# Performance work log

Hardware: AMD Instinct MI355X
Metric: run time of the kernel (lower is better)

The kernel has to match this reference:

```python
import jax, jax.numpy as jnp
import numpy as np

MODEL_DIM = 512
STATE_DIM = 1024
ACTION_DIM = 1000
HEADS = 8
DIM_HEAD = MODEL_DIM // 8      # 64
LANDMARKS = MODEL_DIM // 2     # 256
PINV_ITERS = 6
CONV_K = 33                    # lucidrains residual_conv_kernel default
N_TOKENS = 16383               # seq becomes 16384 after cls token (multiple of LANDMARKS)


def layernorm(x, g, b, eps=1e-5):
    mu = jnp.mean(x, axis=-1, keepdims=True)
    var = jnp.var(x, axis=-1, keepdims=True)
    return (x - mu) * jax.lax.rsqrt(var + eps) * g + b


def moore_penrose_pinv(x, iters=PINV_ITERS):
    # x: [b, h, m, m]
    abs_x = jnp.abs(x)
    col = abs_x.sum(-1)
    row = abs_x.sum(-2)
    z = jnp.swapaxes(x, -1, -2) / (jnp.max(col) * jnp.max(row))
    I = jnp.eye(x.shape[-1], dtype=x.dtype)
    for _ in range(iters):
        xz = x @ z
        z = 0.25 * z @ (13 * I - xz @ (15 * I - xz @ (7 * I - xz)))
    return z


def nystrom_attention(x, qkv_W, conv_W, out_W, out_b):
    # x: [b, n, d]; n divisible by LANDMARKS (no padding branch needed)
    b, n, _ = x.shape
    scale = DIM_HEAD ** -0.5
    qkv = x @ qkv_W                                    # [b, n, 3*h*dh]
    q, k, v = jnp.split(qkv, 3, axis=-1)
    to_heads = lambda t: t.reshape(b, n, HEADS, DIM_HEAD).transpose(0, 2, 1, 3)
    q, k, v = to_heads(q), to_heads(k), to_heads(v)    # [b, h, n, dh]
    q = q * scale
    l = n // LANDMARKS
    q_l = q.reshape(b, HEADS, LANDMARKS, l, DIM_HEAD).mean(3)  # [b,h,m,dh]
    k_l = k.reshape(b, HEADS, LANDMARKS, l, DIM_HEAD).mean(3)
    sim1 = jnp.einsum('bhid,bhjd->bhij', q, k_l)       # [b,h,n,m]
    sim2 = jnp.einsum('bhid,bhjd->bhij', q_l, k_l)     # [b,h,m,m]
    sim3 = jnp.einsum('bhid,bhjd->bhij', q_l, k)       # [b,h,m,n]
    a1 = jax.nn.softmax(sim1, axis=-1)
    a2 = jax.nn.softmax(sim2, axis=-1)
    a3 = jax.nn.softmax(sim3, axis=-1)
    a2_inv = moore_penrose_pinv(a2)
    out = (a1 @ a2_inv) @ (a3 @ v)                     # [b,h,n,dh]
    # residual depthwise conv over sequence dim: treat [b,h,n,dh] as NCHW
    pad = CONV_K // 2
    out = out + jax.lax.conv_general_dilated(
        v, conv_W, window_strides=(1, 1), padding=((pad, pad), (0, 0)),
        dimension_numbers=('NCHW', 'OIHW', 'NCHW'), feature_group_count=HEADS)
    out = out.transpose(0, 2, 1, 3).reshape(b, n, HEADS * DIM_HEAD)
    return out @ out_W + out_b


def trans_layer(h, ln_g, ln_b, qkv_W, conv_W, out_W, out_b):
    # h: [n, d]
    x = h[None]
    x = x + nystrom_attention(layernorm(x, ln_g, ln_b), qkv_W, conv_W, out_W, out_b)
    return x[0]


def setup_inputs() -> dict:
    key = jax.random.key(0)
    ks = jax.random.split(key, 12)
    d = MODEL_DIM
    inp = {
        'h': jax.random.normal(ks[0], (N_TOKENS, STATE_DIM), jnp.float32),
        'W1': jax.random.normal(ks[1], (STATE_DIM, d), jnp.float32) * (STATE_DIM ** -0.5),
        'b1': jnp.zeros((d,), jnp.float32),
        'cls': jax.random.normal(ks[2], (1, d), jnp.float32),
        'ln1_g': jnp.ones((d,), jnp.float32), 'ln1_b': jnp.zeros((d,), jnp.float32),
        'qkv1_W': jax.random.normal(ks[3], (d, 3 * d), jnp.float32) * (d ** -0.5),
        'conv1_W': jax.random.normal(ks[4], (HEADS, 1, CONV_K, 1), jnp.float32) * 0.1,
        'out1_W': jax.random.normal(ks[5], (d, d), jnp.float32) * (d ** -0.5),
        'out1_b': jnp.zeros((d,), jnp.float32),
        'ln2_g': jnp.ones((d,), jnp.float32), 'ln2_b': jnp.zeros((d,), jnp.float32),
        'qkv2_W': jax.random.normal(ks[6], (d, 3 * d), jnp.float32) * (d ** -0.5),
        'conv2_W': jax.random.normal(ks[7], (HEADS, 1, CONV_K, 1), jnp.float32) * 0.1,
        'out2_W': jax.random.normal(ks[8], (d, d), jnp.float32) * (d ** -0.5),
        'out2_b': jnp.zeros((d,), jnp.float32),
        'lnf_g': jnp.ones((d,), jnp.float32), 'lnf_b': jnp.zeros((d,), jnp.float32),
        'fc2_W': jax.random.normal(ks[9], (d, ACTION_DIM), jnp.float32) * (d ** -0.5),
        'fc2_b': jnp.zeros((ACTION_DIM,), jnp.float32),
    }
    return inp


def reference(h, W1, b1, cls, ln1_g, ln1_b, qkv1_W, conv1_W, out1_W, out1_b,
              ln2_g, ln2_b, qkv2_W, conv2_W, out2_W, out2_b,
              lnf_g, lnf_b, fc2_W, fc2_b):
    x = jax.nn.relu(h @ W1 + b1)                 # [N, d]
    x = jnp.concatenate([cls, x], axis=0)        # [N+1, d] (16384)
    x = trans_layer(x, ln1_g, ln1_b, qkv1_W, conv1_W, out1_W, out1_b)
    x = trans_layer(x, ln2_g, ln2_b, qkv2_W, conv2_W, out2_W, out2_b)
    x = layernorm(x, lnf_g, lnf_b)[0]            # cls token
    return x @ fc2_W + fc2_b                     # [action_dim]
```

## Files before the change

kernel.cpp:

```cpp
#include <hip/hip_runtime.h>
#include <math.h>

typedef unsigned short u16;
typedef short bf16x8 __attribute__((ext_vector_type(8)));
typedef float f32x4 __attribute__((ext_vector_type(4)));

__device__ __forceinline__ u16 f2b(float x) {
    unsigned u = __builtin_bit_cast(unsigned, x);
    unsigned r = u + 0x7fffu + ((u >> 16) & 1u);
    return (u16)(r >> 16);
}
__device__ __forceinline__ float b2f(u16 v) {
    return __builtin_bit_cast(float, (unsigned)v << 16);
}
__device__ __forceinline__ void gl_lds16(const u16* g, u16* l) {
    __builtin_amdgcn_global_load_lds(
        (const __attribute__((address_space(1))) unsigned int*)g,
        (__attribute__((address_space(3))) unsigned int*)l, 16, 0, 0);
}
__device__ __forceinline__ float wred_sum(float v) {
#pragma unroll
    for (int o = 32; o > 0; o >>= 1) v += __shfl_down(v, o, 64);
    return v;
}
__device__ __forceinline__ float wred_max(float v) {
#pragma unroll
    for (int o = 32; o > 0; o >>= 1) v = fmaxf(v, __shfl_down(v, o, 64));
    return v;
}

struct GP {
    const u16* A; const u16* B; float* C;
    u16* Q; u16* Kb; u16* V;
    const float* bias;
    long sA, sB, sC;
    int K, ldc, tilesN;
};

template <int BM, int BN, int MODE>
__global__ __launch_bounds__(256) void mgemm(GP p) {
    constexpr int FR = BM / 32;
    constexpr int FC = BN / 32;
    constexpr int LA = BM / 64;
    constexpr int LB = BN / 64;
    __shared__ u16 As[2 * BM * 32] __attribute__((aligned(16)));
    __shared__ u16 Bs[2 * BN * 32] __attribute__((aligned(16)));

    int tid = threadIdx.x, lane = tid & 63, wave = tid >> 6;
    int wm = wave >> 1, wn = wave & 1;
    int nwg = gridDim.x, bid = blockIdx.x;
    int q = nwg >> 3, r = nwg & 7;
    int xcd = bid & 7, local = bid >> 3;
    int swz = (xcd < r ? xcd * (q + 1) : r * (q + 1) + (xcd - r) * q) + local;
    int tm = swz / p.tilesN, tn = swz % p.tilesN;
    int batch = blockIdx.y;
    int m0 = tm * BM, n0 = tn * BN;
    const u16* A = p.A + (long)batch * p.sA;
    const u16* B = p.B + (long)batch * p.sB;

    f32x4 acc[FR][FC];
#pragma unroll
    for (int i = 0; i < FR; i++)
#pragma unroll
        for (int j = 0; j < FC; j++) acc[i][j] = (f32x4){0.f, 0.f, 0.f, 0.f};

    int lr = lane & 15;
    int lcb = (lane >> 4) << 3;
    int quad = lane >> 4, cn = lane & 15;

    auto stage = [&](int buf, int k0) {
        u16* Ad = As + buf * (BM * 32);
        u16* Bd = Bs + buf * (BN * 32);
#pragma unroll
        for (int i = 0; i < LA; i++) {
            int chunk = wave * LA + i;
            gl_lds16(A + (long)(m0 + chunk * 16 + lr) * p.K + k0 + lcb,
                     Ad + chunk * 512 + lane * 8);
        }
#pragma unroll
        for (int i = 0; i < LB; i++) {
            int chunk = wave * LB + i;
            gl_lds16(B + (long)(n0 + chunk * 16 + lr) * p.K + k0 + lcb,
                     Bd + chunk * 512 + lane * 8);
        }
    };

    stage(0, 0);
    __syncthreads();
    int cur = 0;
    for (int k0 = 0; k0 < p.K; k0 += 32) {
        if (k0 + 32 < p.K) stage(cur ^ 1, k0 + 32);
        const u16* Asc = As + cur * (BM * 32);
        const u16* Bsc = Bs + cur * (BN * 32);
        bf16x8 af[FR], bfv[FC];
#pragma unroll
        for (int mi = 0; mi < FR; mi++)
            af[mi] = *(const bf16x8*)(Asc + (wm * FR + mi) * 512 + quad * 128 + cn * 8);
#pragma unroll
        for (int ni = 0; ni < FC; ni++)
            bfv[ni] = *(const bf16x8*)(Bsc + (wn * FC + ni) * 512 + quad * 128 + cn * 8);
#pragma unroll
        for (int mi = 0; mi < FR; mi++)
#pragma unroll
            for (int ni = 0; ni < FC; ni++)
                acc[mi][ni] = __builtin_amdgcn_mfma_f32_16x16x32_bf16(
                    af[mi], bfv[ni], acc[mi][ni], 0, 0, 0);
        __syncthreads();
        cur ^= 1;
    }

    if constexpr (MODE == 4) {
#pragma unroll
        for (int mi = 0; mi < FR; mi++) {
#pragma unroll
            for (int ni = 0; ni < FC; ni++) {
#pragma unroll
                for (int r = 0; r < 4; r++) {
                    int row = m0 + (wm * FR + mi) * 16 + quad * 4 + r;
                    int col = n0 + (wn * FC + ni) * 16 + cn;
                    float v = acc[mi][ni][r];
                    int h = col >> 6, d = col & 63;
                    if (col < 512)
                        p.Q[((long)h * 16384 + row) * 64 + d] = f2b(v * 0.125f);
                    else if (col < 1024)
                        p.Kb[((long)(h - 8) * 16384 + row) * 64 + d] = f2b(v);
                    else
                        p.V[((long)(h - 16) * 16384 + row) * 64 + d] = f2b(v);
                }
            }
        }
    } else {
        float* C = p.C + (long)batch * p.sC;
#pragma unroll
        for (int mi = 0; mi < FR; mi++) {
#pragma unroll
            for (int ni = 0; ni < FC; ni++) {
#pragma unroll
                for (int r = 0; r < 4; r++) {
                    int row = m0 + (wm * FR + mi) * 16 + quad * 4 + r;
                    int col = n0 + (wn * FC + ni) * 16 + cn;
                    float v = acc[mi][ni][r];
                    if (MODE == 0) {
                        C[(long)row * p.ldc + col] = v;
                    } else if (MODE == 1) {
                        C[(long)row * p.ldc + col] = fmaxf(v + p.bias[col], 0.f);
                    } else if (MODE == 2) {
                        C[(long)row * p.ldc + col] += v + p.bias[col];
                    }
                }
            }
        }
    }
}

template <int BM, int BN, int MODE>
static void launch_mgemm(hipStream_t st, GP p, int M, int N, int batch) {
    p.tilesN = N / BN;
    dim3 grid((M / BM) * (N / BN), batch);
    mgemm<BM, BN, MODE><<<grid, 256, 0, st>>>(p);
}

__global__ __launch_bounds__(512) void flash_a3v(
    const u16* __restrict__ QLb, const u16* __restrict__ Kb,
    const u16* __restrict__ VT, float* __restrict__ PART) {
    __shared__ u16 QLs[16384] __attribute__((aligned(16)));
    __shared__ u16 Ks[4096] __attribute__((aligned(16)));
    __shared__ u16 Vs[4096] __attribute__((aligned(16)));
    __shared__ u16 Ps[16384] __attribute__((aligned(16)));
    int tid = threadIdx.x, lane = tid & 63, w = tid >> 6;
    int head = blockIdx.y, split = blockIdx.x;
    const u16* QLh = QLb + (long)head * 256 * 64;
    const u16* Kh = Kb + ((long)head * 16384 + split * 512) * 64;
    const u16* Vh = VT + (long)head * 64 * 16384 + split * 512;
    int quad = lane >> 4, cn = lane & 15;
    int lr = lane & 15, lc = (lane >> 4) << 3;

    for (int c = w; c < 32; c += 8) {
        int rc = c >> 1, kc = c & 1;
        gl_lds16(QLh + (long)(rc * 16 + lr) * 64 + kc * 32 + lc, QLs + c * 512 + lane * 8);
    }
    __syncthreads();
    bf16x8 qf[2][2];
#pragma unroll
    for (int mi = 0; mi < 2; mi++)
#pragma unroll
        for (int kc = 0; kc < 2; kc++)
            qf[mi][kc] = *(const bf16x8*)(QLs + ((w * 2 + mi) * 2 + kc) * 512 +
                                          quad * 128 + cn * 8);

    f32x4 Oacc[2][4];
    float m_i[2][4], l_i[2][4];
#pragma unroll
    for (int i = 0; i < 2; i++)
#pragma unroll
        for (int j = 0; j < 4; j++) {
            Oacc[i][j] = (f32x4){0.f, 0.f, 0.f, 0.f};
            m_i[i][j] = -1e30f;
            l_i[i][j] = 0.f;
        }
#pragma unroll
    for (int i = 0; i < 2; i++)
#pragma unroll
        for (int j = 0; j < 4; j++) {
            m_i[i][j] = -1e30f;
            l_i[i][j] = 0.f;
        }

    for (int t = 0; t < 8; t++) {
        {
            int i = w;
            int rc = i >> 1, kc = i & 1;
            gl_lds16(Kh + (long)(t * 64 + rc * 16 + lr) * 64 + kc * 32 + lc,
                     Ks + i * 512 + lane * 8);
            gl_lds16(Vh + (long)(rc * 16 + lr) * 16384 + t * 64 + kc * 32 + lc,
                     Vs + i * 512 + lane * 8);
        }
        __syncthreads();
        f32x4 s[2][4];
#pragma unroll
        for (int i = 0; i < 2; i++)
#pragma unroll
            for (int j = 0; j < 4; j++) s[i][j] = (f32x4){0.f, 0.f, 0.f, 0.f};
#pragma unroll
        for (int kc = 0; kc < 2; kc++) {
            bf16x8 kf[4];
#pragma unroll
            for (int ni = 0; ni < 4; ni++)
                kf[ni] = *(const bf16x8*)(Ks + (ni * 2 + kc) * 512 + quad * 128 + cn * 8);
#pragma unroll
            for (int mi = 0; mi < 2; mi++)
#pragma unroll
                for (int ni = 0; ni < 4; ni++)
                    s[mi][ni] = __builtin_amdgcn_mfma_f32_16x16x32_bf16(
                        qf[mi][kc], kf[ni], s[mi][ni], 0, 0, 0);
        }
#pragma unroll
        for (int mi = 0; mi < 2; mi++) {
#pragma unroll
            for (int r = 0; r < 4; r++) {
                float mx = fmaxf(fmaxf(s[mi][0][r], s[mi][1][r]),
                                 fmaxf(s[mi][2][r], s[mi][3][r]));
                mx = fmaxf(mx, __shfl_xor(mx, 1));
                mx = fmaxf(mx, __shfl_xor(mx, 2));
                mx = fmaxf(mx, __shfl_xor(mx, 4));
                mx = fmaxf(mx, __shfl_xor(mx, 8));
                float mold = m_i[mi][r];
                float mnew = fmaxf(mold, mx);
                float alpha = __expf(mold - mnew);
                m_i[mi][r] = mnew;
                float sum = 0.f;
#pragma unroll
                for (int ni = 0; ni < 4; ni++) {
                    float e = __expf(s[mi][ni][r] - mnew);
                    sum += e;
                    int col = ni * 16 + cn;
                    Ps[w * 2048 + (mi * 2 + (col >> 5)) * 512 + ((col >> 3) & 3) * 128 +
                       (quad * 4 + r) * 8 + (col & 7)] = f2b(e);
                    Oacc[mi][ni][r] *= alpha;
                }
                sum += __shfl_xor(sum, 1);
                sum += __shfl_xor(sum, 2);
                sum += __shfl_xor(sum, 4);
                sum += __shfl_xor(sum, 8);
                l_i[mi][r] = l_i[mi][r] * alpha + sum;
            }
        }
        __syncthreads();
#pragma unroll
        for (int kc = 0; kc < 2; kc++) {
            bf16x8 vf[4], pf[2];
#pragma unroll
            for (int nd = 0; nd < 4; nd++)
                vf[nd] = *(const bf16x8*)(Vs + (nd * 2 + kc) * 512 + quad * 128 + cn * 8);
#pragma unroll
            for (int mi = 0; mi < 2; mi++)
                pf[mi] = *(const bf16x8*)(Ps + w * 2048 + (mi * 2 + kc) * 512 +
                                          quad * 128 + cn * 8);
#pragma unroll
            for (int mi = 0; mi < 2; mi++)
#pragma unroll
                for (int nd = 0; nd < 4; nd++)
                    Oacc[mi][nd] = __builtin_amdgcn_mfma_f32_16x16x32_bf16(
                        pf[mi], vf[nd], Oacc[mi][nd], 0, 0, 0);
        }
        __syncthreads();
    }
    float* base = PART + ((long)head * 32 + split) * 16896;
#pragma unroll
    for (int mi = 0; mi < 2; mi++) {
#pragma unroll
        for (int r = 0; r < 4; r++) {
            int row = w * 32 + mi * 16 + quad * 4 + r;
            if (cn == 0) {
                base[row] = m_i[mi][r];
                base[256 + row] = l_i[mi][r];
            }
#pragma unroll
            for (int ni = 0; ni < 4; ni++)
                base[512 + row * 64 + ni * 16 + cn] = Oacc[mi][ni][r];
        }
    }
}

__global__ __launch_bounds__(256) void a3v_combine(const float* __restrict__ PART,
                                                   float* __restrict__ O) {
    int head = blockIdx.x, rg = blockIdx.y;
    int t = threadIdx.x;
    int rl = t >> 6, d = t & 63;
    int row = rg * 4 + rl;
    const float* ph = PART + (long)head * 32 * 16896;
    float m = -1e30f;
#pragma unroll 8
    for (int b = 0; b < 32; b++) m = fmaxf(m, ph[b * 16896 + row]);
    float l = 0.f, o = 0.f;
#pragma unroll 8
    for (int b = 0; b < 32; b++) {
        float a = __expf(ph[b * 16896 + row] - m);
        l += a * ph[b * 16896 + 256 + row];
        o += a * ph[b * 16896 + 512 + row * 64 + d];
    }
    O[((long)head * 256 + row) * 64 + d] = o / l;
}

__global__ __launch_bounds__(256) void attn1_fused(
    const u16* __restrict__ Qb, const u16* __restrict__ KLb,
    const u16* __restrict__ W2T, const float* __restrict__ CONV,
    u16* __restrict__ OUTb) {
    __shared__ u16 lds[32768] __attribute__((aligned(16)));
    u16* Qs = lds;
    u16* KLs = lds + 4096;
    u16* Ps = lds;
    u16* W2s = lds + 16384;
    int tid = threadIdx.x, lane = tid & 63, w = tid >> 6;
    int head = blockIdx.y, n0 = blockIdx.x * 64;
    int quad = lane >> 4, cn = lane & 15;
    int lr = lane & 15, lc = (lane >> 4) << 3;
    const u16* Qh = Qb + (long)head * 16384 * 64;
    const u16* KLh = KLb + (long)head * 256 * 64;
    const u16* W2h = W2T + (long)head * 64 * 256;
#pragma unroll
    for (int c = 0; c < 2; c++)
        gl_lds16(Qh + (long)(n0 + w * 16 + lr) * 64 + c * 32 + lc,
                 Qs + c * 2048 + w * 512 + lane * 8);
#pragma unroll
    for (int c = 0; c < 2; c++)
#pragma unroll
        for (int rg = 0; rg < 4; rg++) {
            int chunk = rg * 4 + w;
            gl_lds16(KLh + (long)(chunk * 16 + lr) * 64 + c * 32 + lc,
                     KLs + c * 8192 + chunk * 512 + lane * 8);
        }
    __syncthreads();
    f32x4 acc[16];
#pragma unroll
    for (int i = 0; i < 16; i++) acc[i] = (f32x4){0.f, 0.f, 0.f, 0.f};
#pragma unroll
    for (int c = 0; c < 2; c++) {
        bf16x8 af = *(const bf16x8*)(Qs + c * 2048 + w * 512 + quad * 128 + cn * 8);
#pragma unroll
        for (int ni = 0; ni < 16; ni++) {
            bf16x8 bfv = *(const bf16x8*)(KLs + c * 8192 + ni * 512 + quad * 128 + cn * 8);
            acc[ni] = __builtin_amdgcn_mfma_f32_16x16x32_bf16(af, bfv, acc[ni], 0, 0, 0);
        }
    }
    __syncthreads();
#pragma unroll
    for (int r = 0; r < 4; r++) {
        float mx = -1e30f;
#pragma unroll
        for (int ni = 0; ni < 16; ni++) mx = fmaxf(mx, acc[ni][r]);
        mx = fmaxf(mx, __shfl_xor(mx, 1));
        mx = fmaxf(mx, __shfl_xor(mx, 2));
        mx = fmaxf(mx, __shfl_xor(mx, 4));
        mx = fmaxf(mx, __shfl_xor(mx, 8));
        float e[16];
        float s = 0.f;
#pragma unroll
        for (int ni = 0; ni < 16; ni++) {
            e[ni] = __expf(acc[ni][r] - mx);
            s += e[ni];
        }
        s += __shfl_xor(s, 1);
        s += __shfl_xor(s, 2);
        s += __shfl_xor(s, 4);
        s += __shfl_xor(s, 8);
        float inv = 1.f / s;
        int prow = w * 16 + quad * 4 + r;
#pragma unroll
        for (int ni = 0; ni < 16; ni++) {
            int k = ni * 16 + cn;
            Ps[(k >> 5) * 2048 + ((k >> 3) & 3) * 512 + prow * 8 + (k & 7)] =
                f2b(e[ni] * inv);
        }
    }
#pragma unroll
    for (int c = 0; c < 8; c++)
        gl_lds16(W2h + (long)(w * 16 + lr) * 256 + c * 32 + lc,
                 W2s + c * 2048 + w * 512 + lane * 8);
    __syncthreads();
    f32x4 acc2[4];
#pragma unroll
    for (int i = 0; i < 4; i++) acc2[i] = (f32x4){0.f, 0.f, 0.f, 0.f};
#pragma unroll
    for (int c = 0; c < 8; c++) {
        bf16x8 af = *(const bf16x8*)(Ps + c * 2048 + quad * 512 + (w * 16 + cn) * 8);
#pragma unroll
        for (int ni = 0; ni < 4; ni++) {
            bf16x8 bfv = *(const bf16x8*)(W2s + c * 2048 + ni * 512 + quad * 128 + cn * 8);
            acc2[ni] = __builtin_amdgcn_mfma_f32_16x16x32_bf16(af, bfv, acc2[ni], 0, 0, 0);
        }
    }
#pragma unroll
    for (int ni = 0; ni < 4; ni++)
#pragma unroll
        for (int r = 0; r < 4; r++) {
            int row = n0 + w * 16 + quad * 4 + r;
            long idx = (long)row * 512 + head * 64 + ni * 16 + cn;
            OUTb[idx] = f2b(CONV[idx] + acc2[ni][r]);
        }
}

#define TILE 64
#define KT 16
#define LDP (TILE + 4)
__global__ __launch_bounds__(256) void gemm_kernel(
    const float* __restrict__ A, const float* __restrict__ B, float* __restrict__ C,
    int M, int N, int K, int lda, int ldb, int ldc,
    long sA, long sB, long sC, int tilesN) {
    int tm = blockIdx.x / tilesN, tn = blockIdx.x % tilesN;
    int batch = blockIdx.y;
    A += (long)batch * sA; B += (long)batch * sB; C += (long)batch * sC;
    int row0 = tm * TILE, col0 = tn * TILE;
    __shared__ float As[KT][LDP];
    __shared__ float Bs[KT][LDP];
    int t = threadIdx.x;
    int tx = t & 15, ty = t >> 4;
    float acc[4][4] = {{0.f}};
    int aRow = t >> 2, aK = (t & 3) << 2;
    int bN = t & 63, bK = (t >> 6) << 2;
    for (int k0 = 0; k0 < K; k0 += KT) {
        {
            int r = row0 + aRow;
            float4 av = make_float4(0.f, 0.f, 0.f, 0.f);
            if (r < M) av = *(const float4*)(A + (long)r * lda + k0 + aK);
            As[aK][aRow] = av.x; As[aK + 1][aRow] = av.y;
            As[aK + 2][aRow] = av.z; As[aK + 3][aRow] = av.w;
        }
        {
            const float* bp = B + (long)(k0 + bK) * ldb + col0 + bN;
            bool ok = col0 + bN < N;
#pragma unroll
            for (int j = 0; j < 4; j++) Bs[bK + j][bN] = ok ? bp[(long)j * ldb] : 0.f;
        }
        __syncthreads();
#pragma unroll
        for (int kk = 0; kk < KT; kk++) {
            float4 a = *(const float4*)&As[kk][ty << 2];
            float4 b = *(const float4*)&Bs[kk][tx << 2];
            acc[0][0] += a.x * b.x; acc[0][1] += a.x * b.y; acc[0][2] += a.x * b.z; acc[0][3] += a.x * b.w;
            acc[1][0] += a.y * b.x; acc[1][1] += a.y * b.y; acc[1][2] += a.y * b.z; acc[1][3] += a.y * b.w;
            acc[2][0] += a.z * b.x; acc[2][1] += a.z * b.y; acc[2][2] += a.z * b.z; acc[2][3] += a.z * b.w;
            acc[3][0] += a.w * b.x; acc[3][1] += a.w * b.y; acc[3][2] += a.w * b.z; acc[3][3] += a.w * b.w;
        }
        __syncthreads();
    }
#pragma unroll
    for (int i = 0; i < 4; i++) {
        int row = row0 + (ty << 2) + i;
        if (row >= M) continue;
        float* cp = C + (long)row * ldc + col0 + (tx << 2);
#pragma unroll
        for (int j = 0; j < 4; j++) {
            int col = col0 + (tx << 2) + j;
            if (col >= N) continue;
            cp[j] = acc[i][j];
        }
    }
}
static void gemm32(hipStream_t st, int M, int N, int K,
                   const float* A, int lda, long sA,
                   const float* B, int ldb, long sB,
                   float* C, int ldc, long sC, int batch) {
    int tilesM = (M + TILE - 1) / TILE, tilesN = (N + TILE - 1) / TILE;
    dim3 grid(tilesM * tilesN, batch);
    gemm_kernel<<<grid, 256, 0, st>>>(A, B, C, M, N, K, lda, ldb, ldc, sA, sB, sC, tilesN);
}

__global__ __launch_bounds__(256) void pinv_chain(const float* __restrict__ xz,
                                                  const float* __restrict__ z,
                                                  float* __restrict__ zn,
                                                  u16* __restrict__ znT) {
    int h = blockIdx.y, c0 = blockIdx.x * 8;
    const float* X = xz + (long)h * 65536;
    const float* Z = z + (long)h * 65536;
    __shared__ float ta[256][8];
    __shared__ float tb[256][8];
    int t = threadIdx.x;
    const float4* X4 = (const float4*)(X + t * 256);
    const float4* Z4 = (const float4*)(Z + t * 256);
    float acc[8];
#pragma unroll
    for (int j = 0; j < 8; j++)
        ta[t][j] = ((t == c0 + j) ? 7.f : 0.f) - X[t * 256 + c0 + j];
    __syncthreads();
#pragma unroll
    for (int j = 0; j < 8; j++) acc[j] = 0.f;
    for (int k4 = 0; k4 < 64; k4++) {
        float4 xv = X4[k4];
#pragma unroll
        for (int j = 0; j < 8; j++)
            acc[j] += xv.x * ta[k4 * 4][j] + xv.y * ta[k4 * 4 + 1][j] +
                      xv.z * ta[k4 * 4 + 2][j] + xv.w * ta[k4 * 4 + 3][j];
    }
#pragma unroll
    for (int j = 0; j < 8; j++)
        tb[t][j] = ((t == c0 + j) ? 15.f : 0.f) - acc[j];
    __syncthreads();
#pragma unroll
    for (int j = 0; j < 8; j++) acc[j] = 0.f;
    for (int k4 = 0; k4 < 64; k4++) {
        float4 xv = X4[k4];
#pragma unroll
        for (int j = 0; j < 8; j++)
            acc[j] += xv.x * tb[k4 * 4][j] + xv.y * tb[k4 * 4 + 1][j] +
                      xv.z * tb[k4 * 4 + 2][j] + xv.w * tb[k4 * 4 + 3][j];
    }
    __syncthreads();
#pragma unroll
    for (int j = 0; j < 8; j++)
        ta[t][j] = ((t == c0 + j) ? 13.f : 0.f) - acc[j];
    __syncthreads();
#pragma unroll
    for (int j = 0; j < 8; j++) acc[j] = 0.f;
    for (int k4 = 0; k4 < 64; k4++) {
        float4 zv = Z4[k4];
#pragma unroll
        for (int j = 0; j < 8; j++)
            acc[j] += zv.x * ta[k4 * 4][j] + zv.y * ta[k4 * 4 + 1][j] +
                      zv.z * ta[k4 * 4 + 2][j] + zv.w * ta[k4 * 4 + 3][j];
    }
#pragma unroll
    for (int j = 0; j < 8; j++) {
        float v = 0.25f * acc[j];
        zn[(long)h * 65536 + t * 256 + c0 + j] = v;
        znT[(long)h * 65536 + (c0 + j) * 256 + t] = f2b(v);
    }
}

__global__ __launch_bounds__(256) void layernorm_bf16(
    const float* __restrict__ x, const float* __restrict__ g,
    const float* __restrict__ b, u16* __restrict__ y) {
    __shared__ float sm[4];
    long base = (long)blockIdx.x * 512;
    int t = threadIdx.x;
    float v0 = x[base + t], v1 = x[base + 256 + t];
    float s = wred_sum(v0 + v1);
    if ((t & 63) == 0) sm[t >> 6] = s;
    __syncthreads();
    float mu = (sm[0] + sm[1] + sm[2] + sm[3]) * (1.f / 512.f);
    __syncthreads();
    float d0 = v0 - mu, d1 = v1 - mu;
    float q = wred_sum(d0 * d0 + d1 * d1);
    if ((t & 63) == 0) sm[t >> 6] = q;
    __syncthreads();
    float var = (sm[0] + sm[1] + sm[2] + sm[3]) * (1.f / 512.f);
    float rstd = rsqrtf(var + 1e-5f);
    y[base + t] = f2b(d0 * rstd * g[t] + b[t]);
    y[base + 256 + t] = f2b(d1 * rstd * g[256 + t] + b[256 + t]);
}

__global__ __launch_bounds__(256) void softmax_rows_cs(float* __restrict__ data,
                                                       u16* __restrict__ outb,
                                                       float* __restrict__ colsum) {
    __shared__ float sm[4];
    float* row = data + (long)blockIdx.x * 256;
    u16* rowb = outb + (long)blockIdx.x * 256;
    int h = blockIdx.x >> 8;
    int t = threadIdx.x;
    float v0 = row[t];
    float m = wred_max(v0);
    if ((t & 63) == 0) sm[t >> 6] = m;
    __syncthreads();
    m = fmaxf(fmaxf(sm[0], sm[1]), fmaxf(sm[2], sm[3]));
    __syncthreads();
    float e = __expf(v0 - m);
    float s = wred_sum(e);
    if ((t & 63) == 0) sm[t >> 6] = s;
    __syncthreads();
    s = sm[0] + sm[1] + sm[2] + sm[3];
    float v = e / s;
    row[t] = v;
    rowb[t] = f2b(v);
    atomicAdd(&colsum[h * 256 + t], v);
}

__global__ void cls_copy(const float* __restrict__ cls, float* __restrict__ X) {
    X[threadIdx.x] = cls[threadIdx.x];
}
__global__ void build_hb(const float* __restrict__ h, u16* __restrict__ dst) {
    long idx = (long)blockIdx.x * 256 + threadIdx.x;
    long row = idx >> 10;
    int col = (int)(idx & 1023);
    float v = (row == 0) ? 0.f : h[((row - 1) << 10) + col];
    dst[idx] = f2b(v);
}
__global__ __launch_bounds__(256) void transpose_to_bf16_t(
    const float* __restrict__ src, u16* __restrict__ dst, int R, int C) {
    __shared__ u16 tile[64][65];
    int tilesC = C >> 6;
    int rt = blockIdx.x / tilesC, ct = blockIdx.x % tilesC;
    int t = threadIdx.x, w = t >> 6, lane = t & 63;
    const float* sp = src + (long)(rt * 64) * C + ct * 64;
#pragma unroll
    for (int k = 0; k < 16; k++) {
        int r = w * 16 + k;
        tile[lane][r] = f2b(sp[(long)r * C + lane]);
    }
    __syncthreads();
    u16* dp = dst + (long)(ct * 64) * R + rt * 64;
#pragma unroll
    for (int k = 0; k < 16; k++) {
        int c = w * 16 + k;
        dp[(long)c * R + lane] = tile[c][lane];
    }
}
__global__ __launch_bounds__(256) void transpose_v(const u16* __restrict__ Vb,
                                                   u16* __restrict__ VT) {
    __shared__ u16 tile[64][68];
    int h = blockIdx.y, n0 = blockIdx.x * 64;
    int t = threadIdx.x;
    int i = t >> 2, seg = t & 3;
    const u16* src = Vb + ((long)h * 16384 + n0 + i) * 64 + seg * 16;
#pragma unroll
    for (int j = 0; j < 16; j++) tile[seg * 16 + j][i] = src[j];
    __syncthreads();
    u16* dst = VT + ((long)h * 64 + i) * 16384 + n0 + seg * 16;
#pragma unroll
    for (int j = 0; j < 16; j++) dst[j] = tile[i][seg * 16 + j];
}
__global__ void landmarks_b(const u16* __restrict__ Qb, const u16* __restrict__ Kb,
                            u16* __restrict__ QLb, u16* __restrict__ KLb) {
    int h = blockIdx.x >> 8, j = blockIdx.x & 255, d = threadIdx.x;
    const u16* qb = Qb + ((long)h * 16384 + j * 64) * 64 + d;
    const u16* kb = Kb + ((long)h * 16384 + j * 64) * 64 + d;
    float sq = 0.f, sk = 0.f;
    for (int tk = 0; tk < 64; ++tk) {
        sq += b2f(qb[tk * 64]);
        sk += b2f(kb[tk * 64]);
    }
    QLb[((h << 8) + j) * 64 + d] = f2b(sq * (1.f / 64.f));
    KLb[((h << 8) + j) * 64 + d] = f2b(sk * (1.f / 64.f));
}

__global__ __launch_bounds__(256) void pinv_absmax_fin(const float* __restrict__ colsum,
                                                       float* __restrict__ maxes) {
    __shared__ float sm[4];
    int t = threadIdx.x;
    float m = 0.f;
#pragma unroll
    for (int h = 0; h < 8; h++) m = fmaxf(m, colsum[h * 256 + t]);
    m = wred_max(m);
    if ((t & 63) == 0) sm[t >> 6] = m;
    __syncthreads();
    if (t == 0) {
        maxes[0] = 1.0f;
        maxes[1] = fmaxf(fmaxf(sm[0], sm[1]), fmaxf(sm[2], sm[3]));
    }
}

__global__ void pinv_init(const float* __restrict__ a2, const float* __restrict__ maxes,
                          float* __restrict__ z, u16* __restrict__ zT) {
    long idx = (long)blockIdx.x * 256 + threadIdx.x;
    int h = (int)(idx >> 16);
    int rem = (int)(idx & 65535);
    int i = rem >> 8, j = rem & 255;
    float inv = 1.f / (maxes[0] * maxes[1]);
    float v = a2[((long)h << 16) + (j << 8) + i] * inv;
    z[idx] = v;
    zT[((long)h << 16) + (j << 8) + i] = f2b(v);
}
__global__ __launch_bounds__(256) void conv_kernel(const u16* __restrict__ VT,
                                                   const float* __restrict__ cw,
                                                   float* __restrict__ out) {
    int h = blockIdx.y;
    int n0 = blockIdx.x * 64;
    __shared__ float vt[64][97];
    int t = threadIdx.x;
    for (int i = t; i < 64 * 96; i += 256) {
        int d = i / 96, j = i % 96;
        int n = n0 - 16 + j;
        float v = 0.f;
        if (n >= 0 && n < 16384) v = b2f(VT[((long)h * 64 + d) * 16384 + n]);
        vt[d][j] = v;
    }
    __syncthreads();
    float w[33];
#pragma unroll
    for (int k = 0; k < 33; k++) w[k] = cw[h * 33 + k];
    int d = t & 63, ty = t >> 6;
    for (int nn = 0; nn < 16; nn++) {
        int nl = ty * 16 + nn;
        float s = 0.f;
#pragma unroll
        for (int k = 0; k < 33; k++) s += w[k] * vt[d][nl + k];
        out[((long)(n0 + nl)) * 512 + h * 64 + d] = s;
    }
}
__global__ void w2t_kernel(const float* __restrict__ W2, u16* __restrict__ W2T) {
    int idx = blockIdx.x * 256 + threadIdx.x;
    int h = idx >> 14, rem = idx & 16383, m = rem >> 6, d = rem & 63;
    W2T[(h << 14) + (d << 8) + m] = f2b(W2[idx]);
}
__global__ __launch_bounds__(256) void final_head(
    const float* __restrict__ X, const float* __restrict__ g, const float* __restrict__ b,
    const float* __restrict__ W, const float* __restrict__ bias, float* __restrict__ out) {
    __shared__ float sm[4];
    __shared__ float ln0[512];
    int t = threadIdx.x;
    float v0 = X[t], v1 = X[256 + t];
    float s = wred_sum(v0 + v1);
    if ((t & 63) == 0) sm[t >> 6] = s;
    __syncthreads();
    float mu = (sm[0] + sm[1] + sm[2] + sm[3]) * (1.f / 512.f);
    __syncthreads();
    float d0 = v0 - mu, d1 = v1 - mu;
    float q = wred_sum(d0 * d0 + d1 * d1);
    if ((t & 63) == 0) sm[t >> 6] = q;
    __syncthreads();
    float rstd = rsqrtf((sm[0] + sm[1] + sm[2] + sm[3]) * (1.f / 512.f) + 1e-5f);
    ln0[t] = d0 * rstd * g[t] + b[t];
    ln0[256 + t] = d1 * rstd * g[256 + t] + b[256 + t];
    __syncthreads();
    int jj = blockIdx.x * 256 + t;
    if (jj < 1000) {
        float acc = bias[jj];
        for (int dd = 0; dd < 512; ++dd) acc += ln0[dd] * W[dd * 1000 + jj];
        out[jj] = acc;
    }
}

struct Bufs {
    float *X, *LNA, *A2, *Z0, *Z1, *XZ, *O, *W2, *MAXES, *COLSUM, *PART;
    u16 *LNb, *Qb, *Kb, *Vb, *VT, *QLb, *KLb, *W2T, *W1T, *QKVWT, *OUTWT;
    u16 *A2b, *ZT0, *ZT1;
};

static void run_layer(hipStream_t st, Bufs& B,
                      const float* ln_g, const float* ln_b, const float* qkv_W,
                      const float* conv_W, const float* out_W, const float* out_b) {
    const int N = 16384, D = 512, H = 8, DH = 64, M = 256;
    GP p{};
    layernorm_bf16<<<N, 256, 0, st>>>(B.X, ln_g, ln_b, B.LNb);
    transpose_to_bf16_t<<<(512 / 64) * (1536 / 64), 256, 0, st>>>(qkv_W, B.QKVWT, 512, 1536);
    p = GP{}; p.A = B.LNb; p.B = B.QKVWT; p.Q = B.Qb; p.Kb = B.Kb; p.V = B.Vb; p.K = 512;
    launch_mgemm<128, 128, 4>(st, p, N, 1536, 1);
    transpose_v<<<dim3(256, 8), 256, 0, st>>>(B.Vb, B.VT);
    landmarks_b<<<H * M, 64, 0, st>>>(B.Qb, B.Kb, B.QLb, B.KLb);
    p = GP{}; p.A = B.QLb; p.B = B.KLb; p.C = B.A2; p.K = DH; p.ldc = M;
    p.sA = (long)M * DH; p.sB = (long)M * DH; p.sC = (long)M * M;
    launch_mgemm<64, 64, 0>(st, p, M, M, H);
    hipMemsetAsync(B.COLSUM, 0, 8 * 256 * 4, st);
    softmax_rows_cs<<<H * M, 256, 0, st>>>(B.A2, B.A2b, B.COLSUM);
    pinv_absmax_fin<<<1, 256, 0, st>>>(B.COLSUM, B.MAXES);
    pinv_init<<<(H * M * M) / 256, 256, 0, st>>>(B.A2, B.MAXES, B.Z0, B.ZT0);
    float* z = B.Z0; float* zn = B.Z1;
    u16* zt = B.ZT0; u16* ztn = B.ZT1;
    for (int it = 0; it < 6; ++it) {
        p = GP{}; p.A = B.A2b; p.B = zt; p.C = B.XZ; p.K = M; p.ldc = M;
        p.sA = (long)M * M; p.sB = (long)M * M; p.sC = (long)M * M;
        launch_mgemm<64, 64, 0>(st, p, M, M, H);
        pinv_chain<<<dim3(32, 8), 256, 0, st>>>(B.XZ, z, zn, ztn);
        float* t1 = z; z = zn; zn = t1;
        u16* t2 = zt; zt = ztn; ztn = t2;
    }
    conv_kernel<<<dim3(N / 64, H), 256, 0, st>>>(B.VT, conv_W, B.LNA);
    flash_a3v<<<dim3(32, 8), 512, 0, st>>>(B.QLb, B.Kb, B.VT, B.PART);
    a3v_combine<<<dim3(8, 64), 256, 0, st>>>(B.PART, B.O);
    gemm32(st, M, DH, M, z, M, (long)M * M, B.O, DH, (long)M * DH,
           B.W2, DH, (long)M * DH, H);
    w2t_kernel<<<512, 256, 0, st>>>(B.W2, B.W2T);
    attn1_fused<<<dim3(N / 64, H), 256, 0, st>>>(B.Qb, B.KLb, B.W2T, B.LNA, B.LNb);
    transpose_to_bf16_t<<<(512 / 64) * (512 / 64), 256, 0, st>>>(out_W, B.OUTWT, 512, 512);
    p = GP{}; p.A = B.LNb; p.B = B.OUTWT; p.C = B.X; p.bias = out_b; p.K = D; p.ldc = D;
    launch_mgemm<128, 128, 2>(st, p, N, D, 1);
}

extern "C" void kernel_launch(void* const* d_in, const int* in_sizes, int n_in,
                              void* d_out, int out_size, void* d_ws, size_t ws_size,
                              hipStream_t stream) {
    const float* h_in = (const float*)d_in[0];
    const float* W1 = (const float*)d_in[1];
    const float* b1 = (const float*)d_in[2];
    const float* cls = (const float*)d_in[3];
    const float* ln1_g = (const float*)d_in[4];
    const float* ln1_b = (const float*)d_in[5];
    const float* qkv1_W = (const float*)d_in[6];
    const float* conv1_W = (const float*)d_in[7];
    const float* out1_W = (const float*)d_in[8];
    const float* out1_b = (const float*)d_in[9];
    const float* ln2_g = (const float*)d_in[10];
    const float* ln2_b = (const float*)d_in[11];
    const float* qkv2_W = (const float*)d_in[12];
    const float* conv2_W = (const float*)d_in[13];
    const float* out2_W = (const float*)d_in[14];
    const float* out2_b = (const float*)d_in[15];
    const float* lnf_g = (const float*)d_in[16];
    const float* lnf_b = (const float*)d_in[17];
    const float* fc2_W = (const float*)d_in[18];
    const float* fc2_b = (const float*)d_in[19];
    float* out = (float*)d_out;

    char* wsb = (char*)d_ws;
    size_t off = 0;
    auto alloc = [&](size_t bytes) -> void* {
        void* p = (void*)(wsb + off);
        off += (bytes + 255) & ~(size_t)255;
        return p;
    };
    Bufs B;
    B.X    = (float*)alloc((size_t)16384 * 512 * 4);
    B.LNA  = (float*)alloc((size_t)16384 * 512 * 4);
    B.LNb  = (u16*)alloc((size_t)16384 * 512 * 2);
    B.Qb   = (u16*)alloc((size_t)8 * 16384 * 64 * 2);
    B.Kb   = (u16*)alloc((size_t)8 * 16384 * 64 * 2);
    B.VT   = (u16*)alloc((size_t)8 * 64 * 16384 * 2);
    B.QLb  = (u16*)alloc((size_t)8 * 256 * 64 * 2);
    B.KLb  = (u16*)alloc((size_t)8 * 256 * 64 * 2);
    B.A2   = (float*)alloc((size_t)8 * 256 * 256 * 4);
    B.A2b  = (u16*)alloc((size_t)8 * 256 * 256 * 2);
    B.Z0   = (float*)alloc((size_t)8 * 256 * 256 * 4);
    B.Z1   = (float*)alloc((size_t)8 * 256 * 256 * 4);
    B.ZT0  = (u16*)alloc((size_t)8 * 256 * 256 * 2);
    B.ZT1  = (u16*)alloc((size_t)8 * 256 * 256 * 2);
    B.XZ   = (float*)alloc((size_t)8 * 256 * 256 * 4);
    B.O    = (float*)alloc((size_t)8 * 256 * 64 * 4);
    B.W2   = (float*)alloc((size_t)8 * 256 * 64 * 4);
    B.W2T  = (u16*)alloc((size_t)8 * 64 * 256 * 2);
    B.W1T  = (u16*)alloc((size_t)512 * 1024 * 2);
    B.QKVWT = (u16*)alloc((size_t)1536 * 512 * 2);
    B.OUTWT = (u16*)alloc((size_t)512 * 512 * 2);
    B.MAXES = (float*)alloc(256);
    B.COLSUM = (float*)alloc((size_t)8 * 256 * 4);
    {
        size_t vb = (size_t)8 * 16384 * 64 * 2;
        size_t part = (size_t)8 * 32 * 16896 * 4;
        void* region = alloc(part > vb ? part : vb);
        B.Vb = (u16*)region;
        B.PART = (float*)region;
    }
    if (off > ws_size) return;

    u16* HB = B.Qb;
    build_hb<<<(16384 * 1024) / 256, 256, 0, stream>>>(h_in, HB);
    transpose_to_bf16_t<<<(1024 / 64) * (512 / 64), 256, 0, stream>>>(W1, B.W1T, 1024, 512);
    {
        GP p{}; p.A = HB; p.B = B.W1T; p.C = B.X; p.bias = b1; p.K = 1024; p.ldc = 512;
        launch_mgemm<128, 128, 1>(stream, p, 16384, 512, 1);
    }
    cls_copy<<<1, 512, 0, stream>>>(cls, B.X);

    run_layer(stream, B, ln1_g, ln1_b, qkv1_W, conv1_W, out1_W, out1_b);
    run_layer(stream, B, ln2_g, ln2_b, qkv2_W, conv2_W, out2_W, out2_b);

    final_head<<<4, 256, 0, stream>>>(B.X, lnf_g, lnf_b, fc2_W, fc2_b, out);
}
```

Before: 1.281 ms.

## Add single-shot LDS GEMM for small pinv matmuls and widen pinv_chain to 512 threads

Adds sgemm_one, a 64x64-tile MFMA GEMM that loads the entire K extent (up to 256) into LDS in one pass and then runs the MFMA loop with no further synchronisation. It replaces the generic mgemm for the landmark sim2 product and for the x@z product in each pinv iteration. pinv_chain now runs 512 threads per block, each computing 4 columns instead of 8, which doubles the threads working on these small, latency-bound kernels. The cost is higher LDS use per block (64 KB) and twice as many redundant row loads of X and Z in pinv_chain.

```diff
diff --git a/kernel.cpp b/kernel.cpp
--- a/kernel.cpp
+++ b/kernel.cpp
@@ -158,6 +158,63 @@
     p.tilesN = N / BN;
     dim3 grid((M / BM) * (N / BN), batch);
     mgemm<BM, BN, MODE><<<grid, 256, 0, st>>>(p);
+}
+
+__global__ __launch_bounds__(256) void sgemm_one(GP p) {
+    __shared__ u16 As[64 * 256] __attribute__((aligned(16)));
+    __shared__ u16 Bs[64 * 256] __attribute__((aligned(16)));
+    int tid = threadIdx.x, lane = tid & 63, wave = tid >> 6;
+    int wm = wave >> 1, wn = wave & 1;
+    int tm = blockIdx.x / p.tilesN, tn = blockIdx.x % p.tilesN;
+    int batch = blockIdx.y;
+    int m0 = tm * 64, n0 = tn * 64;
+    const u16* A = p.A + (long)batch * p.sA;
+    const u16* B = p.B + (long)batch * p.sB;
+    int lr = lane & 15, lcb = (lane >> 4) << 3;
+    int quad = lane >> 4, cn = lane & 15;
+    int nseg = p.K >> 5;
+    for (int rc = 0; rc < 4; rc++)
+        for (int ks = wave; ks < nseg; ks += 4) {
+            int c = rc * nseg + ks;
+            gl_lds16(A + (long)(m0 + rc * 16 + lr) * p.K + ks * 32 + lcb,
+                     As + c * 512 + lane * 8);
+            gl_lds16(B + (long)(n0 + rc * 16 + lr) * p.K + ks * 32 + lcb,
+                     Bs + c * 512 + lane * 8);
+        }
+    __syncthreads();
+    f32x4 acc[2][2];
+#pragma unroll
+    for (int i = 0; i < 2; i++)
+#pragma unroll
+        for (int j = 0; j < 2; j++) acc[i][j] = (f32x4){0.f, 0.f, 0.f, 0.f};
+    for (int ks = 0; ks < nseg; ks++) {
+        bf16x8 af[2], bfv[2];
+#pragma unroll
+        for (int mi = 0; mi < 2; mi++)
+            af[mi] = *(const bf16x8*)(As + ((wm * 2 + mi) * nseg + ks) * 512 +
+                                      quad * 128 + cn * 8);
+#pragma unroll
+        for (int ni = 0; ni < 2; ni++)
+            bfv[ni] = *(const bf16x8*)(Bs + ((wn * 2 + ni) * nseg + ks) * 512 +
+                                       quad * 128 + cn * 8);
+#pragma unroll
+        for (int mi = 0; mi < 2; mi++)
+#pragma unroll
+            for (int ni = 0; ni < 2; ni++)
+                acc[mi][ni] = __builtin_amdgcn_mfma_f32_16x16x32_bf16(
+                    af[mi], bfv[ni], acc[mi][ni], 0, 0, 0);
+    }
+    float* C = p.C + (long)batch * p.sC;
+#pragma unroll
+    for (int mi = 0; mi < 2; mi++)
+#pragma unroll
+        for (int ni = 0; ni < 2; ni++)
+#pragma unroll
+            for (int r = 0; r < 4; r++) {
+                int row = m0 + (wm * 2 + mi) * 16 + quad * 4 + r;
+                int col = n0 + (wn * 2 + ni) * 16 + cn;
+                C[(long)row * p.ldc + col] = acc[mi][ni][r];
+            }
 }
 
 __global__ __launch_bounds__(512) void flash_a3v(
@@ -195,13 +252,6 @@
 #pragma unroll
         for (int j = 0; j < 4; j++) {
             Oacc[i][j] = (f32x4){0.f, 0.f, 0.f, 0.f};
-            m_i[i][j] = -1e30f;
-            l_i[i][j] = 0.f;
-        }
-#pragma unroll
-    for (int i = 0; i < 2; i++)
-#pragma unroll
-        for (int j = 0; j < 4; j++) {
             m_i[i][j] = -1e30f;
             l_i[i][j] = 0.f;
         }
@@ -486,7 +536,7 @@
     gemm_kernel<<<grid, 256, 0, st>>>(A, B, C, M, N, K, lda, ldb, ldc, sA, sB, sC, tilesN);
 }
 
-__global__ __launch_bounds__(256) void pinv_chain(const float* __restrict__ xz,
+__global__ __launch_bounds__(512) void pinv_chain(const float* __restrict__ xz,
                                                   const float* __restrict__ z,
                                                   float* __restrict__ zn,
                                                   u16* __restrict__ znT) {
@@ -495,55 +545,56 @@
     const float* Z = z + (long)h * 65536;
     __shared__ float ta[256][8];
     __shared__ float tb[256][8];
-    int t = threadIdx.x;
+    int tid = threadIdx.x;
+    int t = tid & 255, cb = (tid >> 8) << 2;
     const float4* X4 = (const float4*)(X + t * 256);
     const float4* Z4 = (const float4*)(Z + t * 256);
-    float acc[8];
-#pragma unroll
-    for (int j = 0; j < 8; j++)
-        ta[t][j] = ((t == c0 + j) ? 7.f : 0.f) - X[t * 256 + c0 + j];
-    __syncthreads();
-#pragma unroll
-    for (int j = 0; j < 8; j++) acc[j] = 0.f;
+    float acc[4];
+#pragma unroll
+    for (int j = 0; j < 4; j++)
+        ta[t][cb + j] = ((t == c0 + cb + j) ? 7.f : 0.f) - X[t * 256 + c0 + cb + j];
+    __syncthreads();
+#pragma unroll
+    for (int j = 0; j < 4; j++) acc[j] = 0.f;
     for (int k4 = 0; k4 < 64; k4++) {
         float4 xv = X4[k4];
 #pragma unroll
-        for (int j = 0; j < 8; j++)
-            acc[j] += xv.x * ta[k4 * 4][j] + xv.y * ta[k4 * 4 + 1][j] +
-                      xv.z * ta[k4 * 4 + 2][j] + xv.w * ta[k4 * 4 + 3][j];
-    }
-#pragma unroll
-    for (int j = 0; j < 8; j++)
-        tb[t][j] = ((t == c0 + j) ? 15.f : 0.f) - acc[j];
-    __syncthreads();
-#pragma unroll
-    for (int j = 0; j < 8; j++) acc[j] = 0.f;
+        for (int j = 0; j < 4; j++)
+            acc[j] += xv.x * ta[k4 * 4][cb + j] + xv.y * ta[k4 * 4 + 1][cb + j] +
+                      xv.z * ta[k4 * 4 + 2][cb + j] + xv.w * ta[k4 * 4 + 3][cb + j];
+    }
+#pragma unroll
+    for (int j = 0; j < 4; j++)
+        tb[t][cb + j] = ((t == c0 + cb + j) ? 15.f : 0.f) - acc[j];
+    __syncthreads();
+#pragma unroll
+    for (int j = 0; j < 4; j++) acc[j] = 0.f;
     for (int k4 = 0; k4 < 64; k4++) {
         float4 xv = X4[k4];
 #pragma unroll
-        for (int j = 0; j < 8; j++)
-            acc[j] += xv.x * tb[k4 * 4][j] + xv.y * tb[k4 * 4 + 1][j] +
-                      xv.z * tb[k4 * 4 + 2][j] + xv.w * tb[k4 * 4 + 3][j];
-    }
-    __syncthreads();
-#pragma unroll
-    for (int j = 0; j < 8; j++)
-        ta[t][j] = ((t == c0 + j) ? 13.f : 0.f) - acc[j];
-    __syncthreads();
-#pragma unroll
-    for (int j = 0; j < 8; j++) acc[j] = 0.f;
+        for (int j = 0; j < 4; j++)
+            acc[j] += xv.x * tb[k4 * 4][cb + j] + xv.y * tb[k4 * 4 + 1][cb + j] +
+                      xv.z * tb[k4 * 4 + 2][cb + j] + xv.w * tb[k4 * 4 + 3][cb + j];
+    }
+    __syncthreads();
+#pragma unroll
+    for (int j = 0; j < 4; j++)
+        ta[t][cb + j] = ((t == c0 + cb + j) ? 13.f : 0.f) - acc[j];
+    __syncthreads();
+#pragma unroll
+    for (int j = 0; j < 4; j++) acc[j] = 0.f;
     for (int k4 = 0; k4 < 64; k4++) {
         float4 zv = Z4[k4];
 #pragma unroll
-        for (int j = 0; j < 8; j++)
-            acc[j] += zv.x * ta[k4 * 4][j] + zv.y * ta[k4 * 4 + 1][j] +
-                      zv.z * ta[k4 * 4 + 2][j] + zv.w * ta[k4 * 4 + 3][j];
-    }
-#pragma unroll
-    for (int j = 0; j < 8; j++) {
+        for (int j = 0; j < 4; j++)
+            acc[j] += zv.x * ta[k4 * 4][cb + j] + zv.y * ta[k4 * 4 + 1][cb + j] +
+                      zv.z * ta[k4 * 4 + 2][cb + j] + zv.w * ta[k4 * 4 + 3][cb + j];
+    }
+#pragma unroll
+    for (int j = 0; j < 4; j++) {
         float v = 0.25f * acc[j];
-        zn[(long)h * 65536 + t * 256 + c0 + j] = v;
-        znT[(long)h * 65536 + (c0 + j) * 256 + t] = f2b(v);
+        zn[(long)h * 65536 + t * 256 + c0 + cb + j] = v;
+        znT[(long)h * 65536 + (c0 + cb + j) * 256 + t] = f2b(v);
     }
 }
 
@@ -758,7 +809,8 @@
     landmarks_b<<<H * M, 64, 0, st>>>(B.Qb, B.Kb, B.QLb, B.KLb);
     p = GP{}; p.A = B.QLb; p.B = B.KLb; p.C = B.A2; p.K = DH; p.ldc = M;
     p.sA = (long)M * DH; p.sB = (long)M * DH; p.sC = (long)M * M;
-    launch_mgemm<64, 64, 0>(st, p, M, M, H);
+    p.tilesN = 4;
+    sgemm_one<<<dim3(16, H), 256, 0, st>>>(p);
     hipMemsetAsync(B.COLSUM, 0, 8 * 256 * 4, st);
     softmax_rows_cs<<<H * M, 256, 0, st>>>(B.A2, B.A2b, B.COLSUM);
     pinv_absmax_fin<<<1, 256, 0, st>>>(B.COLSUM, B.MAXES);
@@ -768,8 +820,9 @@
     for (int it = 0; it < 6; ++it) {
         p = GP{}; p.A = B.A2b; p.B = zt; p.C = B.XZ; p.K = M; p.ldc = M;
         p.sA = (long)M * M; p.sB = (long)M * M; p.sC = (long)M * M;
-        launch_mgemm<64, 64, 0>(st, p, M, M, H);
-        pinv_chain<<<dim3(32, 8), 256, 0, st>>>(B.XZ, z, zn, ztn);
+        p.tilesN = 4;
+        sgemm_one<<<dim3(16, H), 256, 0, st>>>(p);
+        pinv_chain<<<dim3(32, 8), 512, 0, st>>>(B.XZ, z, zn, ztn);
         float* t1 = z; z = zn; zn = t1;
         u16* t2 = zt; zt = ztn; ztn = t2;
     }
```

Measured after the change: 1.481 ms. 1.16x slower.
